# Kernel optimization log

Hardware: AMD Instinct MI355X
Metric: run time of the kernel (lower is better)

## Reference

```python
import jax, jax.numpy as jnp
import numpy as np

DECAY = 0.99
EPS = 1e-05


def setup_inputs() -> dict:
    key = jax.random.key(0)
    k1, k2 = jax.random.split(key)
    x = jax.random.normal(k1, (32, 2048, 128), dtype=jnp.float32)
    embed = jax.random.normal(k2, (1024, 128), dtype=jnp.float32)
    cluster_size = jnp.zeros((1024,), dtype=jnp.float32)
    embed_avg = embed  # register_buffer('embed_avg', embed.clone())
    return {"x": x, "embed": embed, "cluster_size": cluster_size, "embed_avg": embed_avg}


def reference(x, embed, cluster_size, embed_avg):
    N, D = embed.shape
    flat_x = x.reshape(-1, D)  # [T, D]
    distances = (
        jnp.sum(flat_x * flat_x, axis=1, keepdims=True)
        + jnp.sum(embed * embed, axis=1)
        - 2.0 * flat_x @ embed.T
    )  # [T, N]
    idx = jnp.argmin(distances, axis=1)  # [T]
    quantized = embed[idx].reshape(x.shape)
    # EMA codebook update (training branch); segment_sum replaces the one-hot matmuls
    counts = jax.ops.segment_sum(jnp.ones(flat_x.shape[0], dtype=x.dtype), idx, num_segments=N)
    embed_sums = jax.ops.segment_sum(flat_x, idx, num_segments=N)  # [N, D]
    new_cluster_size = DECAY * cluster_size + (1.0 - DECAY) * counts
    new_embed_avg = DECAY * embed_avg + (1.0 - DECAY) * embed_sums
    n = jnp.sum(new_cluster_size)
    cs = (new_cluster_size + EPS) / (n + N * EPS) * n
    new_embed = new_embed_avg / cs[:, None]
    # straight-through estimator
    out = x + jax.lax.stop_gradient(quantized - x)
    return out, new_embed, new_cluster_size, new_embed_avg
```

## Files before the change

### kernel.cpp

```cpp
#include <hip/hip_runtime.h>

#define NTOK   65536
#define NCODES 1024
#define DIM    128
#define BT     64
#define MARGIN 6.0f
#define CAP    960

typedef __attribute__((ext_vector_type(8))) short short8;
typedef __attribute__((ext_vector_type(4))) float f32x4;
typedef const __attribute__((address_space(1))) char gchar_t;
typedef __attribute__((address_space(3))) char lchar_t;

__device__ __forceinline__ unsigned short f2bf(float f) {
  unsigned u = __float_as_uint(f);
  u += 0x7FFFu + ((u >> 16) & 1u);
  return (unsigned short)(u >> 16);
}

__global__ __launch_bounds__(256) void prep_kernel(const float* __restrict__ E,
                                                   float* __restrict__ ee,
                                                   unsigned short* __restrict__ ebf,
                                                   float* __restrict__ zero_base) {
  #pragma clang fp contract(off)
  const int b = blockIdx.x;
  if (b < 64) {
    const int id = b * 256 + threadIdx.x;
    const int l  = id & 63;
    const int s  = (id >> 6) & 3;
    const int ct = id >> 8;
    const int c  = ct * 16 + (l & 15);
    const int ko = s * 32 + (l >> 4) * 8;
    const float4* p = (const float4*)(E + (size_t)c * DIM + ko);
    float4 A = p[0], B = p[1];
    short8 v;
    v[0]=f2bf(A.x); v[1]=f2bf(A.y); v[2]=f2bf(A.z); v[3]=f2bf(A.w);
    v[4]=f2bf(B.x); v[5]=f2bf(B.y); v[6]=f2bf(B.z); v[7]=f2bf(B.w);
    ((short8*)ebf)[id] = v;
  } else if (b < 68) {
    const int c = (b - 64) * 256 + threadIdx.x;
    const float4* r4 = (const float4*)(E + (size_t)c * DIM);
    float v[DIM];
    #pragma unroll
    for (int i = 0; i < 32; ++i) {
      float4 q = r4[i];
      v[4*i] = q.x; v[4*i+1] = q.y; v[4*i+2] = q.z; v[4*i+3] = q.w;
    }
    float r[8];
    #pragma unroll
    for (int j = 0; j < 8; ++j) r[j] = v[j] * v[j];
    #pragma unroll
    for (int i = 1; i < 16; ++i) {
      #pragma unroll
      for (int j = 0; j < 8; ++j) { float s = v[8*i+j] * v[8*i+j]; r[j] = r[j] + s; }
    }
    ee[c] = ((r[0]+r[1])+(r[2]+r[3])) + ((r[4]+r[5])+(r[6]+r[7]));
  } else {
    float4 z = {0.f, 0.f, 0.f, 0.f};
    ((float4*)zero_base)[(b - 68) * 256 + threadIdx.x] = z;
  }
}

__global__ __launch_bounds__(256, 4) void vq_main(
    const float* __restrict__ X, const float* __restrict__ E,
    const unsigned short* __restrict__ ebf, const float* __restrict__ ee,
    float* __restrict__ out, int* __restrict__ idxg, int* __restrict__ cnt_i) {
  #pragma clang fp contract(off)
  __shared__ __align__(16) char e_lds[4 * 8192];
  __shared__ __align__(16) unsigned short eebf[NCODES];
  __shared__ __align__(16) float bestA[4][BT];
  __shared__ __align__(16) float thrf[BT];
  __shared__ __align__(16) unsigned long long best64[BT];
  __shared__ int cand_n;
  __shared__ unsigned cand[CAP];

  const int tid  = threadIdx.x;
  const int lane = tid & 63;
  const int wv   = tid >> 6;
  const int bid  = blockIdx.x;
  const long blk = (bid & 7) * 128 + (bid >> 3);
  const float* Xb = X + (size_t)blk * BT * DIM;

  {
    float4 e4 = *((const float4*)ee + tid);
    eebf[tid * 4 + 0] = f2bf(e4.x);
    eebf[tid * 4 + 1] = f2bf(e4.y);
    eebf[tid * 4 + 2] = f2bf(e4.z);
    eebf[tid * 4 + 3] = f2bf(e4.w);
  }

  short8 afr[4][4];
  #pragma unroll
  for (int tt = 0; tt < 4; ++tt) {
    const int row = tt * 16 + (lane & 15);
    #pragma unroll
    for (int s = 0; s < 4; ++s) {
      const float4* p = (const float4*)(Xb + row * DIM + (s * 4 + (lane >> 4)) * 8);
      float4 A = p[0], B = p[1];
      short8 v;
      v[0]=f2bf(A.x); v[1]=f2bf(A.y); v[2]=f2bf(A.z); v[3]=f2bf(A.w);
      v[4]=f2bf(B.x); v[5]=f2bf(B.y); v[6]=f2bf(B.z); v[7]=f2bf(B.w);
      afr[tt][s] = v;
    }
  }

  char* myl = e_lds + wv * 8192;
#define STAGE(CT, BUF)                                                        \
  { _Pragma("unroll")                                                         \
    for (int s = 0; s < 4; ++s) {                                             \
      gchar_t* src = (gchar_t*)((const char*)ebf                              \
          + ((size_t)((((wv * 16 + (CT)) * 4 + s) * 64) + lane) << 4));       \
      lchar_t* dst = (lchar_t*)(myl + (BUF) * 4096 + s * 1024);               \
      __builtin_amdgcn_global_load_lds(                                       \
          (const __attribute__((address_space(1))) void*)src,                 \
          (__attribute__((address_space(3))) void*)dst, 16, 0, 0);            \
    } }

#define MFMA4(ACC, TT)                                                        \
  ACC = __builtin_amdgcn_mfma_f32_16x16x32_bf16(afr[TT][0], b0, ACC, 0, 0, 0);\
  ACC = __builtin_amdgcn_mfma_f32_16x16x32_bf16(afr[TT][1], b1, ACC, 0, 0, 0);\
  ACC = __builtin_amdgcn_mfma_f32_16x16x32_bf16(afr[TT][2], b2, ACC, 0, 0, 0);\
  ACC = __builtin_amdgcn_mfma_f32_16x16x32_bf16(afr[TT][3], b3, ACC, 0, 0, 0);

  STAGE(0, 0)
  __syncthreads();

  float bv[4][4];
  #pragma unroll
  for (int tt = 0; tt < 4; ++tt)
    #pragma unroll
    for (int rg = 0; rg < 4; ++rg) bv[tt][rg] = __builtin_inff();

  for (int ct = 0; ct < 16; ++ct) {
    STAGE((ct + 1) & 15, (ct + 1) & 1)
    asm volatile("s_waitcnt vmcnt(4)" ::: "memory");
    const char* eb = myl + (ct & 1) * 4096;
    short8 b0 = *(const short8*)(eb +    0 + lane * 16);
    short8 b1 = *(const short8*)(eb + 1024 + lane * 16);
    short8 b2 = *(const short8*)(eb + 2048 + lane * 16);
    short8 b3 = *(const short8*)(eb + 3072 + lane * 16);
    const unsigned short eu = eebf[(wv * 16 + ct) * 16 + (lane & 15)];
    const float ev = __uint_as_float((unsigned)eu << 16);
    #pragma unroll
    for (int tt = 0; tt < 4; ++tt) {
      f32x4 acc = {0.f, 0.f, 0.f, 0.f};
      MFMA4(acc, tt)
      #pragma unroll
      for (int rg = 0; rg < 4; ++rg) {
        float d = ev - 2.0f * acc[rg];
        if (d < bv[tt][rg]) bv[tt][rg] = d;
      }
    }
  }

  #pragma unroll
  for (int tt = 0; tt < 4; ++tt)
    #pragma unroll
    for (int rg = 0; rg < 4; ++rg) {
      float b = bv[tt][rg];
      #pragma unroll
      for (int m = 1; m < 16; m <<= 1) {
        float pb = __shfl_xor(b, m, 64);
        if (pb < b) b = pb;
      }
      if ((lane & 15) == 0)
        bestA[wv][tt * 16 + (lane >> 4) * 4 + rg] = b;
    }
  __syncthreads();

  if (tid < BT) {
    float m0 = bestA[0][tid], m1 = bestA[1][tid];
    float m2 = bestA[2][tid], m3 = bestA[3][tid];
    thrf[tid]   = fminf(fminf(m0, m1), fminf(m2, m3)) + MARGIN;
    best64[tid] = ~0ull;
  }
  if (tid == 0) cand_n = 0;
  __syncthreads();

  float thv[4][4];
  #pragma unroll
  for (int tt = 0; tt < 4; ++tt)
    #pragma unroll
    for (int rg = 0; rg < 4; ++rg)
      thv[tt][rg] = thrf[tt * 16 + (lane >> 4) * 4 + rg];

  for (int ct = 0; ct < 16; ++ct) {
    STAGE((ct + 1) & 15, (ct + 1) & 1)
    asm volatile("s_waitcnt vmcnt(4)" ::: "memory");
    const char* eb = myl + (ct & 1) * 4096;
    short8 b0 = *(const short8*)(eb +    0 + lane * 16);
    short8 b1 = *(const short8*)(eb + 1024 + lane * 16);
    short8 b2 = *(const short8*)(eb + 2048 + lane * 16);
    short8 b3 = *(const short8*)(eb + 3072 + lane * 16);
    const int code = (wv * 16 + ct) * 16 + (lane & 15);
    const unsigned short eu = eebf[code];
    const float ev = __uint_as_float((unsigned)eu << 16);
    #pragma unroll
    for (int tt = 0; tt < 4; ++tt) {
      f32x4 acc = {0.f, 0.f, 0.f, 0.f};
      MFMA4(acc, tt)
      #pragma unroll
      for (int rg = 0; rg < 4; ++rg) {
        float d = ev - 2.0f * acc[rg];
        if (d < thv[tt][rg]) {
          int sl = atomicAdd(&cand_n, 1);
          if (sl < CAP)
            cand[sl] = ((unsigned)(tt * 16 + (lane >> 4) * 4 + rg) << 10)
                     | (unsigned)code;
        }
      }
    }
  }
  __syncthreads();

  {
    int cn = cand_n;
    const int nc = cn < CAP ? cn : CAP;
    for (int i = tid; i < nc; i += 256) {
      const unsigned pc = cand[i];
      const int t = pc >> 10, c = pc & 1023;
      const float* xr = Xb + t * DIM;
      const float* er = E + (size_t)c * DIM;
      float dot = 0.0f;
      #pragma unroll
      for (int k = 0; k < DIM; ++k) dot = __builtin_fmaf(xr[k], er[k], dot);
      float d = ee[c] - 2.0f * dot;
      unsigned u = __float_as_uint(d);
      u ^= (unsigned)((int)u >> 31) | 0x80000000u;
      unsigned long long key = ((unsigned long long)u << 32) | (unsigned)c;
      atomicMin(best64 + t, key);
    }
  }
  __syncthreads();

  if (tid < BT) {
    const int c0 = (int)(best64[tid] & 1023ull);
    idxg[blk * BT + tid] = c0;
    atomicAdd(cnt_i + c0, 1);
  }
  const int tt2 = tid >> 2, hf = tid & 3;
  const int fi2 = (int)(best64[tt2] & 1023ull);
  const float* xrow = Xb  + tt2 * DIM + hf * 32;
  const float* erow = E   + ((size_t)fi2 << 7) + hf * 32;
  float*       orow = out + ((size_t)blk * BT + tt2) * DIM + hf * 32;
  #pragma unroll
  for (int q = 0; q < 8; ++q) {
    float4 xv = *(const float4*)(xrow + q * 4);
    float4 ev = *(const float4*)(erow + q * 4);
    float4 o;
    o.x = xv.x + (ev.x - xv.x);
    o.y = xv.y + (ev.y - xv.y);
    o.z = xv.z + (ev.z - xv.z);
    o.w = xv.w + (ev.w - xv.w);
    *(float4*)(orow + q * 4) = o;
  }
}

__global__ __launch_bounds__(1024) void prefix_fin1(
    const float* __restrict__ cluster_size, const int* __restrict__ cnt_i,
    float* __restrict__ out_cs, float* __restrict__ cs_ws,
    int* __restrict__ cursor, int* __restrict__ offs) {
  #pragma clang fp contract(off)
  __shared__ float red[1024];
  __shared__ int   sc[1024];
  const int n = threadIdx.x;
  const int cnt = cnt_i[n];
  float ncs = 0.99f * cluster_size[n] + 0.01f * (float)cnt;
  out_cs[n] = ncs;
  red[n] = ncs;
  sc[n]  = cnt;
  __syncthreads();
  for (int s = 512; s > 0; s >>= 1) {
    if (n < s) red[n] = red[n] + red[n + s];
    __syncthreads();
  }
  float ntot = red[0];
  cs_ws[n] = (ncs + 1e-5f) / (ntot + 0.01024f) * ntot;
  for (int d = 1; d < 1024; d <<= 1) {
    int t = (n >= d) ? sc[n - d] : 0;
    __syncthreads();
    sc[n] += t;
    __syncthreads();
  }
  int excl = sc[n] - cnt;
  cursor[n] = excl;
  offs[n]   = excl;
}

__global__ __launch_bounds__(256) void scatter_kernel(
    const int* __restrict__ idxg, int* __restrict__ cursor,
    int* __restrict__ order) {
  const int t  = blockIdx.x * 256 + threadIdx.x;
  const int fi = idxg[t];
  const int slot = atomicAdd(cursor + fi, 1);
  order[slot] = t;
}

__global__ __launch_bounds__(256) void sums_chunk(
    const float* __restrict__ X, const int* __restrict__ order,
    const int* __restrict__ idxg, float* __restrict__ sums) {
  #pragma clang fp contract(off)
  const int lane = threadIdx.x & 63;
  const int base = blockIdx.x * 256 + (threadIdx.x >> 6) * 64;
  const int tl = order[base + lane];
  const int cl = idxg[tl];
  float ax = 0.f, ay = 0.f;
  int cprev = __shfl(cl, 0, 64);
  #pragma unroll
  for (int j0 = 0; j0 < 64; j0 += 8) {
    int tj[8], cj[8];
    float2 buf[8];
    #pragma unroll
    for (int q = 0; q < 8; ++q) tj[q] = __shfl(tl, j0 + q, 64);
    #pragma unroll
    for (int q = 0; q < 8; ++q)
      buf[q] = *((const float2*)(X + ((size_t)tj[q] << 7)) + lane);
    #pragma unroll
    for (int q = 0; q < 8; ++q) cj[q] = __shfl(cl, j0 + q, 64);
    #pragma unroll
    for (int q = 0; q < 8; ++q) {
      if (cj[q] != cprev) {
        atomicAdd(sums + cprev * DIM + lane * 2,     ax);
        atomicAdd(sums + cprev * DIM + lane * 2 + 1, ay);
        ax = 0.f; ay = 0.f; cprev = cj[q];
      }
      ax = ax + buf[q].x;
      ay = ay + buf[q].y;
    }
  }
  atomicAdd(sums + cprev * DIM + lane * 2,     ax);
  atomicAdd(sums + cprev * DIM + lane * 2 + 1, ay);
}

__global__ __launch_bounds__(256) void finalize2(
    const float* __restrict__ embed_avg, const float* __restrict__ sums,
    const float* __restrict__ cs_ws, float* __restrict__ out_embed,
    float* __restrict__ out_avg) {
  #pragma clang fp contract(off)
  int i = blockIdx.x * 256 + threadIdx.x;
  float av = 0.99f * embed_avg[i] + 0.01f * sums[i];
  out_avg[i]   = av;
  out_embed[i] = av / cs_ws[i >> 7];
}

extern "C" void kernel_launch(void* const* d_in, const int* in_sizes, int n_in,
                              void* d_out, int out_size, void* d_ws, size_t ws_size,
                              hipStream_t stream) {
  const float* X  = (const float*)d_in[0];
  const float* E  = (const float*)d_in[1];
  const float* CS = (const float*)d_in[2];
  const float* EA = (const float*)d_in[3];
  float* out = (float*)d_out;
  float* ws  = (float*)d_ws;

  int*   cnt_i  = (int*)ws;
  float* sums   = ws + 1024;
  float* eearr  = ws + 132096;
  float* csarr  = ws + 133120;
  int*   cursor = (int*)(ws + 134144);
  int*   offs   = (int*)(ws + 135168);
  int*   idxarr = (int*)(ws + 136192);
  int*   order  = (int*)(ws + 201728);
  unsigned short* ebf = (unsigned short*)(ws + 267264);

  prep_kernel   <<<197,          256, 0, stream>>>(E, eearr, ebf, ws);
  vq_main       <<<NTOK / BT,    256, 0, stream>>>(X, E, ebf, eearr, out,
                                                   idxarr, cnt_i);
  prefix_fin1   <<<1, 1024, 0, stream>>>(CS, cnt_i, out + 8519680, csarr,
                                         cursor, offs);
  scatter_kernel<<<NTOK / 256,   256, 0, stream>>>(idxarr, cursor, order);
  sums_chunk    <<<NTOK / 256,   256, 0, stream>>>(X, order, idxarr, sums);
  finalize2     <<<131072 / 256, 256, 0, stream>>>(EA, sums, csarr,
                                                   out + 8388608, out + 8520704);
}
```

Before: 159.5 us.

## Replace two-pass block threshold with per-wave running min and 1.5 codebook passes

Instead of a full first pass over all codes followed by a block-wide min reduction and a second full pass, each wave computes a partial minimum over its first half of codes, derives a per-wave threshold with margin, then emits candidates over the remaining half and re-scans the first half. This removes two block barriers, the LDS eebf/bestA/thrf arrays and a quarter of the MFMA work, and keeps ee values packed in registers. In exchange, thresholds come from half the codebook per wave, so more candidates are produced; CAP is raised to compensate and the exact rescoring loop is vectorised with float4 loads. MFMA issue priority is also raised via s_setprio.

```diff
diff --git a/kernel.cpp b/kernel.cpp
--- a/kernel.cpp
+++ b/kernel.cpp
@@ -5,7 +5,7 @@
 #define DIM    128
 #define BT     64
 #define MARGIN 6.0f
-#define CAP    960
+#define CAP    1791
 
 typedef __attribute__((ext_vector_type(8))) short short8;
 typedef __attribute__((ext_vector_type(4))) float f32x4;
@@ -67,9 +67,6 @@
     float* __restrict__ out, int* __restrict__ idxg, int* __restrict__ cnt_i) {
   #pragma clang fp contract(off)
   __shared__ __align__(16) char e_lds[4 * 8192];
-  __shared__ __align__(16) unsigned short eebf[NCODES];
-  __shared__ __align__(16) float bestA[4][BT];
-  __shared__ __align__(16) float thrf[BT];
   __shared__ __align__(16) unsigned long long best64[BT];
   __shared__ int cand_n;
   __shared__ unsigned cand[CAP];
@@ -81,13 +78,8 @@
   const long blk = (bid & 7) * 128 + (bid >> 3);
   const float* Xb = X + (size_t)blk * BT * DIM;
 
-  {
-    float4 e4 = *((const float4*)ee + tid);
-    eebf[tid * 4 + 0] = f2bf(e4.x);
-    eebf[tid * 4 + 1] = f2bf(e4.y);
-    eebf[tid * 4 + 2] = f2bf(e4.z);
-    eebf[tid * 4 + 3] = f2bf(e4.w);
-  }
+  if (tid < BT) best64[tid] = ~0ull;
+  if (tid == 0) cand_n = 0;
 
   short8 afr[4][4];
   #pragma unroll
@@ -102,6 +94,14 @@
       v[4]=f2bf(B.x); v[5]=f2bf(B.y); v[6]=f2bf(B.z); v[7]=f2bf(B.w);
       afr[tt][s] = v;
     }
+  }
+
+  unsigned eevp[8];
+  #pragma unroll
+  for (int j = 0; j < 8; ++j) {
+    float e0 = ee[(wv * 16 + 2 * j)     * 16 + (lane & 15)];
+    float e1 = ee[(wv * 16 + 2 * j + 1) * 16 + (lane & 15)];
+    eevp[j] = (unsigned)f2bf(e0) | ((unsigned)f2bf(e1) << 16);
   }
 
   char* myl = e_lds + wv * 8192;
@@ -122,94 +122,75 @@
   ACC = __builtin_amdgcn_mfma_f32_16x16x32_bf16(afr[TT][2], b2, ACC, 0, 0, 0);\
   ACC = __builtin_amdgcn_mfma_f32_16x16x32_bf16(afr[TT][3], b3, ACC, 0, 0, 0);
 
+#define CHUNK_HEAD(I, GUARD)                                                  \
+    if (GUARD) STAGE(((I) + 1) & 15, ((I) + 1) & 1)                           \
+    asm volatile("s_waitcnt vmcnt(4)" ::: "memory");                          \
+    const char* eb = myl + ((I) & 1) * 4096;                                  \
+    short8 b0 = *(const short8*)(eb +    0 + lane * 16);                      \
+    short8 b1 = *(const short8*)(eb + 1024 + lane * 16);                      \
+    short8 b2 = *(const short8*)(eb + 2048 + lane * 16);                      \
+    short8 b3 = *(const short8*)(eb + 3072 + lane * 16);                      \
+    const int ctk = (I) & 15;                                                 \
+    const unsigned ep = eevp[ctk >> 1];                                       \
+    const float ev = __uint_as_float((ctk & 1) ? (ep & 0xffff0000u)           \
+                                               : (ep << 16));                 \
+    __builtin_amdgcn_s_setprio(1);                                            \
+    f32x4 a0 = {0,0,0,0}, a1 = {0,0,0,0}, a2 = {0,0,0,0}, a3 = {0,0,0,0};     \
+    { MFMA4(a0, 0) } { MFMA4(a1, 1) } { MFMA4(a2, 2) } { MFMA4(a3, 3) }       \
+    __builtin_amdgcn_s_setprio(0);
+
+#define PROC_MIN(ACC, TT)                                                     \
+  { _Pragma("unroll") for (int rg = 0; rg < 4; ++rg) {                        \
+      float d = __builtin_fmaf(-2.0f, ACC[rg], ev);                           \
+      if (d < thv[TT][rg]) thv[TT][rg] = d; } }
+
+#define PROC_EMIT(ACC, TT)                                                    \
+  { _Pragma("unroll") for (int rg = 0; rg < 4; ++rg) {                        \
+      float d = __builtin_fmaf(-2.0f, ACC[rg], ev);                           \
+      if (d < thv[TT][rg]) {                                                  \
+        int sl = atomicAdd(&cand_n, 1);                                       \
+        if (sl < CAP)                                                         \
+          cand[sl] = ((unsigned)((TT) * 16 + (lane >> 4) * 4 + rg) << 10)     \
+                   | (unsigned)(((wv * 16 + ctk) << 4) + (lane & 15)); } } }
+
+  float thv[4][4];
+  #pragma unroll
+  for (int tt = 0; tt < 4; ++tt)
+    #pragma unroll
+    for (int rg = 0; rg < 4; ++rg) thv[tt][rg] = __builtin_inff();
+
   STAGE(0, 0)
   __syncthreads();
 
-  float bv[4][4];
+  #pragma unroll 2
+  for (int i = 0; i < 8; ++i) {
+    CHUNK_HEAD(i, 1)
+    PROC_MIN(a0, 0) PROC_MIN(a1, 1) PROC_MIN(a2, 2) PROC_MIN(a3, 3)
+  }
+
   #pragma unroll
   for (int tt = 0; tt < 4; ++tt)
     #pragma unroll
-    for (int rg = 0; rg < 4; ++rg) bv[tt][rg] = __builtin_inff();
-
-  for (int ct = 0; ct < 16; ++ct) {
-    STAGE((ct + 1) & 15, (ct + 1) & 1)
-    asm volatile("s_waitcnt vmcnt(4)" ::: "memory");
-    const char* eb = myl + (ct & 1) * 4096;
-    short8 b0 = *(const short8*)(eb +    0 + lane * 16);
-    short8 b1 = *(const short8*)(eb + 1024 + lane * 16);
-    short8 b2 = *(const short8*)(eb + 2048 + lane * 16);
-    short8 b3 = *(const short8*)(eb + 3072 + lane * 16);
-    const unsigned short eu = eebf[(wv * 16 + ct) * 16 + (lane & 15)];
-    const float ev = __uint_as_float((unsigned)eu << 16);
-    #pragma unroll
-    for (int tt = 0; tt < 4; ++tt) {
-      f32x4 acc = {0.f, 0.f, 0.f, 0.f};
-      MFMA4(acc, tt)
-      #pragma unroll
-      for (int rg = 0; rg < 4; ++rg) {
-        float d = ev - 2.0f * acc[rg];
-        if (d < bv[tt][rg]) bv[tt][rg] = d;
-      }
-    }
-  }
-
-  #pragma unroll
-  for (int tt = 0; tt < 4; ++tt)
-    #pragma unroll
     for (int rg = 0; rg < 4; ++rg) {
-      float b = bv[tt][rg];
+      float b = thv[tt][rg];
       #pragma unroll
       for (int m = 1; m < 16; m <<= 1) {
         float pb = __shfl_xor(b, m, 64);
         if (pb < b) b = pb;
       }
-      if ((lane & 15) == 0)
-        bestA[wv][tt * 16 + (lane >> 4) * 4 + rg] = b;
-    }
-  __syncthreads();
-
-  if (tid < BT) {
-    float m0 = bestA[0][tid], m1 = bestA[1][tid];
-    float m2 = bestA[2][tid], m3 = bestA[3][tid];
-    thrf[tid]   = fminf(fminf(m0, m1), fminf(m2, m3)) + MARGIN;
-    best64[tid] = ~0ull;
-  }
-  if (tid == 0) cand_n = 0;
-  __syncthreads();
-
-  float thv[4][4];
-  #pragma unroll
-  for (int tt = 0; tt < 4; ++tt)
-    #pragma unroll
-    for (int rg = 0; rg < 4; ++rg)
-      thv[tt][rg] = thrf[tt * 16 + (lane >> 4) * 4 + rg];
-
-  for (int ct = 0; ct < 16; ++ct) {
-    STAGE((ct + 1) & 15, (ct + 1) & 1)
-    asm volatile("s_waitcnt vmcnt(4)" ::: "memory");
-    const char* eb = myl + (ct & 1) * 4096;
-    short8 b0 = *(const short8*)(eb +    0 + lane * 16);
-    short8 b1 = *(const short8*)(eb + 1024 + lane * 16);
-    short8 b2 = *(const short8*)(eb + 2048 + lane * 16);
-    short8 b3 = *(const short8*)(eb + 3072 + lane * 16);
-    const int code = (wv * 16 + ct) * 16 + (lane & 15);
-    const unsigned short eu = eebf[code];
-    const float ev = __uint_as_float((unsigned)eu << 16);
-    #pragma unroll
-    for (int tt = 0; tt < 4; ++tt) {
-      f32x4 acc = {0.f, 0.f, 0.f, 0.f};
-      MFMA4(acc, tt)
-      #pragma unroll
-      for (int rg = 0; rg < 4; ++rg) {
-        float d = ev - 2.0f * acc[rg];
-        if (d < thv[tt][rg]) {
-          int sl = atomicAdd(&cand_n, 1);
-          if (sl < CAP)
-            cand[sl] = ((unsigned)(tt * 16 + (lane >> 4) * 4 + rg) << 10)
-                     | (unsigned)code;
-        }
-      }
-    }
+      thv[tt][rg] = b + MARGIN;
+    }
+
+  #pragma unroll 2
+  for (int i = 8; i < 16; ++i) {
+    CHUNK_HEAD(i, 1)
+    PROC_EMIT(a0, 0) PROC_EMIT(a1, 1) PROC_EMIT(a2, 2) PROC_EMIT(a3, 3)
+  }
+
+  #pragma unroll 2
+  for (int i = 16; i < 24; ++i) {
+    CHUNK_HEAD(i, i < 23)
+    PROC_EMIT(a0, 0) PROC_EMIT(a1, 1) PROC_EMIT(a2, 2) PROC_EMIT(a3, 3)
   }
   __syncthreads();
 
@@ -219,11 +200,18 @@
     for (int i = tid; i < nc; i += 256) {
       const unsigned pc = cand[i];
       const int t = pc >> 10, c = pc & 1023;
-      const float* xr = Xb + t * DIM;
-      const float* er = E + (size_t)c * DIM;
+      const float4* xr = (const float4*)(Xb + t * DIM);
+      const float4* er = (const float4*)(E + (size_t)c * DIM);
       float dot = 0.0f;
       #pragma unroll
-      for (int k = 0; k < DIM; ++k) dot = __builtin_fmaf(xr[k], er[k], dot);
+      for (int k4 = 0; k4 < 32; ++k4) {
+        float4 xv = xr[k4];
+        float4 ev4 = er[k4];
+        dot = __builtin_fmaf(xv.x, ev4.x, dot);
+        dot = __builtin_fmaf(xv.y, ev4.y, dot);
+        dot = __builtin_fmaf(xv.z, ev4.z, dot);
+        dot = __builtin_fmaf(xv.w, ev4.w, dot);
+      }
       float d = ee[c] - 2.0f * dot;
       unsigned u = __float_as_uint(d);
       u ^= (unsigned)((int)u >> 31) | 0x80000000u;
```

New measurement: 270.4 us. 1.69x slower.
